# Optimization experiments

Measured on AMD Instinct MI355X. Metric: run time of the kernel, lower is better.

Reference implementation:

```python
import jax, jax.numpy as jnp
import numpy as np
import math

DIM, HEADS, WS, RED = 192, 6, 7, 4
HD = DIM // HEADS
N = WS * WS
BW = 4096  # total windows (B_)


def _pdsca(x, ca_w1, ca_b1, ca_w2, ca_b2, sa_w, sa_b):
    # Parallel dual channel+spatial attention producing mask logits, same shape as x.
    # x: (B, C, 7, 7)
    ca = x.mean(axis=(2, 3))                              # (B, C) global avg pool
    h = jax.nn.gelu(ca @ ca_w1.T + ca_b1)                 # (B, C/r)
    ca = h @ ca_w2.T + ca_b2                              # (B, C)
    sa_in = jnp.concatenate([x.mean(axis=1, keepdims=True),
                             x.max(axis=1, keepdims=True)], axis=1)  # (B, 2, 7, 7)
    sa = jax.lax.conv_general_dilated(sa_in, sa_w, (1, 1), 'SAME',
                                      dimension_numbers=('NCHW', 'OIHW', 'NCHW'))
    sa = sa + sa_b[None, :, None, None]                   # (B, 1, 7, 7)
    return ca[:, :, None, None] + sa                      # broadcast to (B, C, 7, 7)


def _forward(qkv, log_temp, pos_w, pos_b, pos_scale,
             meta_w1, meta_b1, meta_w2, meta_b2,
             q_ca_w1, q_ca_b1, q_ca_w2, q_ca_b2, q_sa_w, q_sa_b,
             k_ca_w1, k_ca_b1, k_ca_w2, k_ca_b2, k_sa_w, k_sa_b,
             proj_w):
    B = qkv.shape[0]
    qkv5 = qkv.reshape(B, N, 3, HEADS, HD).transpose(2, 0, 3, 1, 4)  # (3, B, H, N, hd)
    q, k, v = qkv5[0], qkv5[1], qkv5[2]

    temperature = jnp.exp(log_temp)

    # sigmoid gates on q and k via PDSCA on (B*H, hd, 7, 7) windows
    mq = _pdsca(q.reshape(-1, HD, WS, WS), q_ca_w1, q_ca_b1, q_ca_w2, q_ca_b2, q_sa_w, q_sa_b)
    mk = _pdsca(k.reshape(-1, HD, WS, WS), k_ca_w1, k_ca_b1, k_ca_w2, k_ca_b2, k_sa_w, k_sa_b)
    q = q * jax.nn.sigmoid(mq.reshape(q.shape))
    k = k * jax.nn.sigmoid(mk.reshape(k.shape))

    attn = jnp.einsum('bhnd,bhmd->bhnm', q, k) * temperature  # (B, H, N, N)

    # learned relative position bias: conv1x1 on coord grid -> pairwise diffs -> meta MLP
    coords = jnp.linspace(-1.0, 1.0, WS)
    yg, xg = jnp.meshgrid(coords, coords, indexing='ij')
    grid = jnp.stack([xg, yg], axis=0)                        # (2, 7, 7)
    pe = jnp.einsum('chw,dc->dhw', grid, pos_w) + pos_b[:, None, None]  # (dim, 7, 7)
    pef = pe.reshape(DIM, N).T                                # (N, dim)
    rel = pos_scale * (pef[:, None, :] - pef[None, :, :])     # (N, N, dim)
    bias = jax.nn.gelu(rel @ meta_w1 + meta_b1) @ meta_w2 + meta_b2  # (N, N, H)
    bias = bias.transpose(2, 0, 1)                            # (H, N, N)

    attn = jax.nn.softmax(attn + bias[None], axis=-1)
    out = jnp.einsum('bhnm,bhmd->bnhd', attn, v).reshape(B, N, DIM)
    return out @ proj_w.T                                     # project_out 1x1 conv


def setup_inputs() -> dict:
    key = jax.random.key(0)
    ks = jax.random.split(key, 24)
    s = 0.02
    d = {
        'qkv': jax.random.normal(ks[0], (BW, N, 3 * DIM), dtype=jnp.float32),
        'log_temp': jnp.array([math.log(0.1)], dtype=jnp.float32),
        'pos_w': jax.random.normal(ks[1], (DIM, 2), dtype=jnp.float32) * s,
        'pos_b': jnp.zeros((DIM,), dtype=jnp.float32),
        'pos_scale': jnp.float32(0.1),
        'meta_w1': jax.random.normal(ks[2], (DIM, 128), dtype=jnp.float32) * s,
        'meta_b1': jnp.zeros((128,), dtype=jnp.float32),
        'meta_w2': jax.random.normal(ks[3], (128, HEADS), dtype=jnp.float32) * s,
        'meta_b2': jnp.zeros((HEADS,), dtype=jnp.float32),
        'q_ca_w1': jax.random.normal(ks[4], (HD // RED, HD), dtype=jnp.float32) * s,
        'q_ca_b1': jnp.zeros((HD // RED,), dtype=jnp.float32),
        'q_ca_w2': jax.random.normal(ks[5], (HD, HD // RED), dtype=jnp.float32) * s,
        'q_ca_b2': jnp.zeros((HD,), dtype=jnp.float32),
        'q_sa_w': jax.random.normal(ks[6], (1, 2, 7, 7), dtype=jnp.float32) * s,
        'q_sa_b': jnp.zeros((1,), dtype=jnp.float32),
        'k_ca_w1': jax.random.normal(ks[7], (HD // RED, HD), dtype=jnp.float32) * s,
        'k_ca_b1': jnp.zeros((HD // RED,), dtype=jnp.float32),
        'k_ca_w2': jax.random.normal(ks[8], (HD, HD // RED), dtype=jnp.float32) * s,
        'k_ca_b2': jnp.zeros((HD,), dtype=jnp.float32),
        'k_sa_w': jax.random.normal(ks[9], (1, 2, 7, 7), dtype=jnp.float32) * s,
        'k_sa_b': jnp.zeros((1,), dtype=jnp.float32),
        'proj_w': jax.random.normal(ks[10], (DIM, DIM), dtype=jnp.float32) * s,
    }
    return d


def reference(qkv, log_temp, pos_w, pos_b, pos_scale,
              meta_w1, meta_b1, meta_w2, meta_b2,
              q_ca_w1, q_ca_b1, q_ca_w2, q_ca_b2, q_sa_w, q_sa_b,
              k_ca_w1, k_ca_b1, k_ca_w2, k_ca_b2, k_sa_w, k_sa_b,
              proj_w):
    return _forward(qkv, log_temp, pos_w, pos_b, pos_scale,
                    meta_w1, meta_b1, meta_w2, meta_b2,
                    q_ca_w1, q_ca_b1, q_ca_w2, q_ca_b2, q_sa_w, q_sa_b,
                    k_ca_w1, k_ca_b1, k_ca_w2, k_ca_b2, k_sa_w, k_sa_b,
                    proj_w)
```

## Files before the change

kernel.cpp:

```cpp
#include <hip/hip_runtime.h>
#include <math.h>

#define DIM 192
#define HEADS 6
#define HD 32
#define WS 7
#define NN 49
#define NWIN 4096
#define QKV_ROW (3*DIM)

typedef __attribute__((ext_vector_type(8))) short bf16x8_t;
typedef __attribute__((ext_vector_type(4))) float f32x4_t;

#define MFMA16(a,b,c) __builtin_amdgcn_mfma_f32_16x16x32_bf16((a),(b),(c),0,0,0)

__device__ __forceinline__ float gelu_tanh(float x) {
    const float k0 = 0.7978845608028654f;
    const float k1 = 0.044715f;
    float t = tanhf(k0 * (x + k1 * x * x * x));
    return 0.5f * x * (1.0f + t);
}
__device__ __forceinline__ unsigned short f2bf(float f) {
    __bf16 h = (__bf16)f;
    return __builtin_bit_cast(unsigned short, h);
}
__device__ __forceinline__ float bf2f(unsigned short u) {
    return (float)__builtin_bit_cast(__bf16, u);
}

#define BIASF_FLOATS (HEADS*64*64)
#define WBF_OFF_B    (BIASF_FLOATS*4)
#define OWS_OFF_B    (WBF_OFF_B + DIM*DIM*2)
#define WS_NEEDED    ((size_t)OWS_OFF_B + (size_t)NWIN*HEADS*NN*HD*2)

__global__ __launch_bounds__(128) void bias_kernel(
    const float* __restrict__ pos_w, const float* __restrict__ pos_scale,
    const float* __restrict__ meta_w1, const float* __restrict__ meta_b1,
    const float* __restrict__ meta_w2, const float* __restrict__ meta_b2,
    float* __restrict__ bias_frag)
{
    const int p = blockIdx.x;
    const int n = p / NN, m = p % NN;
    const int i = threadIdx.x;
    __shared__ float hbuf[128];
    const float step = 2.0f / 6.0f;
    const float dx = (float)((n % WS) - (m % WS)) * step;
    const float dy = (float)((n / WS) - (m / WS)) * step;
    const float ps = pos_scale[0];
    float a = meta_b1[i];
    for (int d = 0; d < DIM; ++d) {
        float rel = ps * (pos_w[2*d] * dx + pos_w[2*d+1] * dy);
        a += rel * meta_w1[d*128 + i];
    }
    hbuf[i] = gelu_tanh(a);
    __syncthreads();
    if (i < HEADS) {
        float b = meta_b2[i];
        for (int j = 0; j < 128; ++j) b += hbuf[j] * meta_w2[j*HEADS + i];
        bias_frag[((i*64 + n)*16 + (m & 15))*4 + (m >> 4)] = b;
    }
}

__global__ __launch_bounds__(256) void prep_w(
    const float* __restrict__ proj_w, unsigned short* __restrict__ wbf,
    float* __restrict__ bias_frag)
{
    int idx = blockIdx.x*256 + threadIdx.x;
    if (idx < DIM*DIM) wbf[idx] = f2bf(proj_w[idx]);
    int z = idx - DIM*DIM;
    if (z >= 0 && z < HEADS*15*64) {
        int hh = z / 960, rem = z - hh*960;
        int row = 49 + (rem >> 6), inner = rem & 63;
        bias_frag[(hh*64 + row)*64 + inner] = 0.f;
    }
}

#define XS  40
#define VS  72
#define PPS 72

#define G_SM 0
#define G_MX 49
#define G_CA 98
#define G_SA 130

__device__ __forceinline__ void stats_one(
    const unsigned short* xs,
    const float* __restrict__ w1, const float* __restrict__ b1,
    const float* __restrict__ w2, const float* __restrict__ b2,
    const float* sw, float sab, float* scr, int l)
{
    int c = l & 31, h2 = l >> 5;
    int s0 = h2 ? 25 : 0, s1 = h2 ? 49 : 25;
    float s = 0.f;
    for (int sp = s0; sp < s1; ++sp) {
        int j = c*NN + sp;
        s += bf2f(xs[(j >> 5)*XS + (j & 31)]);
    }
    s += __shfl_xor(s, 32);
    float cm = s * (1.f/49.f);
    int o = l & 7, t8 = l >> 3;
    float part = 0.f;
    #pragma unroll
    for (int kk = 0; kk < 4; ++kk) {
        int c2 = t8 + (kk << 3);
        part += w1[(o << 5) + c2] * __shfl(cm, c2);
    }
    part += __shfl_xor(part, 8);
    part += __shfl_xor(part, 16);
    part += __shfl_xor(part, 32);
    float hid = gelu_tanh(part + b1[o]);
    float a2 = b2[c];
    #pragma unroll
    for (int oo = 0; oo < 8; ++oo)
        a2 += w2[(c << 3) + oo] * __shfl(hid, oo);
    scr[G_CA + c] = a2;
    if (l < NN) {
        float sm = 0.f, mx = -1e30f;
        #pragma unroll
        for (int c2 = 0; c2 < HD; ++c2) {
            int j2 = c2*NN + l;
            float v = bf2f(xs[(j2 >> 5)*XS + (j2 & 31)]);
            sm += v; mx = fmaxf(mx, v);
        }
        scr[G_SM + l] = sm * (1.f/HD);
        scr[G_MX + l] = mx;
        int y = l / WS, x = l - y*WS;
        int y0 = max(0, y-3), y1 = min(6, y+3);
        int x0 = max(0, x-3), x1 = min(6, x+3);
        float a = sab;
        for (int iy = y0; iy <= y1; ++iy) {
            int ky = iy - y + 3;
            for (int ix = x0; ix <= x1; ++ix) {
                int kx = ix - x + 3;
                int s2 = iy*WS + ix;
                a += sw[ky*WS+kx] * scr[G_SM+s2] + sw[NN+ky*WS+kx] * scr[G_MX+s2];
            }
        }
        scr[G_SA + l] = a;
    }
}

__device__ __forceinline__ bf16x8_t gate_frag(
    const unsigned short* xs, int row, int lk8, const float* scr)
{
    bf16x8_t r = *(const bf16x8_t*)&xs[row*XS + lk8];
    bf16x8_t g;
    int flat = row*HD + lk8;
    int c = flat / NN, sp = flat - c*NN;
    #pragma unroll
    for (int e = 0; e < 8; ++e) {
        float gg = __fdividef(1.f, 1.f + __expf(-(scr[G_CA+c] + scr[G_SA+sp])));
        g[e] = (short)f2bf(bf2f((unsigned short)r[e]) * gg);
        if (++sp >= NN) { sp = 0; ++c; }
    }
    return g;
}

__global__ __launch_bounds__(128) void gate_attn(
    const float* __restrict__ qkv,
    const float* __restrict__ log_temp,
    const float* __restrict__ q_ca_w1, const float* __restrict__ q_ca_b1,
    const float* __restrict__ q_ca_w2, const float* __restrict__ q_ca_b2,
    const float* __restrict__ q_sa_w, const float* __restrict__ q_sa_b,
    const float* __restrict__ k_ca_w1, const float* __restrict__ k_ca_b1,
    const float* __restrict__ k_ca_w2, const float* __restrict__ k_ca_b2,
    const float* __restrict__ k_sa_w, const float* __restrict__ k_sa_b,
    const float* __restrict__ bias_frag,
    unsigned short* __restrict__ o_ws)
{
    __shared__ __align__(16) unsigned short x_all[2][NN*XS];
    __shared__ __align__(16) unsigned short v_all[2][HD*VS];
    __shared__ __align__(16) unsigned short p_all[2][16*PPS];
    __shared__ __align__(16) float sw_s[196];

    const int t = threadIdx.x;
    const int w = t >> 6;
    const int l = t & 63;
    const int lrow = l & 15;
    const int lk = l >> 4;
    const int lk8 = lk * 8;
    const int u = blockIdx.x*2 + w;
    const int b = u / HEADS;
    const int h = u - b*HEADS;
    const int hoff = h * HD;
    unsigned short* x_buf = x_all[w];
    unsigned short* v_t = v_all[w];
    unsigned short* p_buf = p_all[w];
    float* scr = (float*)p_buf;
    const float temp = __expf(log_temp[0]);
    const float* qkv_b = qkv + (size_t)b * (NN*QKV_ROW);

    for (int i = l; i < 196; i += 64)
        sw_s[i] = (i < 98) ? q_sa_w[i] : k_sa_w[i-98];
    for (int i = l; i < HD*15; i += 64) {
        int d = i / 15, m = 49 + (i - d*15);
        v_t[d*VS + m] = 0;
    }

    #pragma unroll
    for (int i = 0; i < 7; ++i) {
        int e = l + i*64;
        if (e < NN*8) {
            int n = e >> 3, c = e & 7;
            const float* base = qkv_b + n*QKV_ROW + hoff + (c<<2);
            float4 fv = *(const float4*)(base + 2*DIM);
            float4 fq = *(const float4*)(base);
            int d0 = c << 2;
            v_t[(d0+0)*VS + n] = f2bf(fv.x);
            v_t[(d0+1)*VS + n] = f2bf(fv.y);
            v_t[(d0+2)*VS + n] = f2bf(fv.z);
            v_t[(d0+3)*VS + n] = f2bf(fv.w);
            ushort4 uq = { f2bf(fq.x), f2bf(fq.y), f2bf(fq.z), f2bf(fq.w) };
            *(ushort4*)&x_buf[n*XS + (c<<2)] = uq;
        }
    }

    stats_one(x_buf, q_ca_w1, q_ca_b1, q_ca_w2, q_ca_b2, sw_s, q_sa_b[0], scr, l);
    bf16x8_t qfrag[4];
    #pragma unroll
    for (int s = 0; s < 4; ++s) {
        int ar = s*16 + lrow;
        qfrag[s] = gate_frag(x_buf, ar < NN ? ar : NN-1, lk8, scr);
    }

    #pragma unroll
    for (int i = 0; i < 7; ++i) {
        int e = l + i*64;
        if (e < NN*8) {
            int n = e >> 3, c = e & 7;
            float4 fk = *(const float4*)(qkv_b + n*QKV_ROW + DIM + hoff + (c<<2));
            ushort4 uk = { f2bf(fk.x), f2bf(fk.y), f2bf(fk.z), f2bf(fk.w) };
            *(ushort4*)&x_buf[n*XS + (c<<2)] = uk;
        }
    }

    stats_one(x_buf, k_ca_w1, k_ca_b1, k_ca_w2, k_ca_b2, sw_s + 98, k_sa_b[0], scr, l);
    {
        int c2 = l / NN, sp = l - c2*NN;
        for (int j = l; j < NN*HD; j += 64) {
            int idx = (j >> 5)*XS + (j & 31);
            float g = __fdividef(1.f, 1.f + __expf(-(scr[G_CA+c2] + scr[G_SA+sp])));
            x_buf[idx] = f2bf(bf2f(x_buf[idx]) * g);
            sp += 15; c2 += 1;
            if (sp >= NN) { sp -= NN; ++c2; }
        }
    }

    const float* bias_f = bias_frag + h*64*64;
    unsigned short* o_u = o_ws + (size_t)u * (NN*HD);
    #pragma unroll
    for (int s = 0; s < 4; ++s) {
        f32x4_t sac[4];
        #pragma unroll
        for (int j = 0; j < 4; ++j) {
            int mr = j*16 + lrow;
            int mc = mr < NN ? mr : NN-1;
            bf16x8_t bk = *(const bf16x8_t*)&x_buf[mc*XS + lk8];
            f32x4_t z = (f32x4_t){0.f,0.f,0.f,0.f};
            sac[j] = MFMA16(qfrag[s], bk, z);
        }
        #pragma unroll
        for (int r = 0; r < 4; ++r) {
            int row = s*16 + lk*4 + r;
            float4 b4 = *(const float4*)(bias_f + (row*16 + lrow)*4);
            float v0 = sac[0][r]*temp + b4.x;
            float v1 = sac[1][r]*temp + b4.y;
            float v2 = sac[2][r]*temp + b4.z;
            float v3 = (lrow == 0) ? (sac[3][r]*temp + b4.w) : -1e30f;
            float mx = fmaxf(fmaxf(v0, v1), fmaxf(v2, v3));
            mx = fmaxf(mx, __shfl_xor(mx, 1));
            mx = fmaxf(mx, __shfl_xor(mx, 2));
            mx = fmaxf(mx, __shfl_xor(mx, 4));
            mx = fmaxf(mx, __shfl_xor(mx, 8));
            float e0 = __expf(v0 - mx), e1 = __expf(v1 - mx);
            float e2 = __expf(v2 - mx), e3 = __expf(v3 - mx);
            float sum = e0 + e1 + e2 + e3;
            sum += __shfl_xor(sum, 1);
            sum += __shfl_xor(sum, 2);
            sum += __shfl_xor(sum, 4);
            sum += __shfl_xor(sum, 8);
            float inv = __fdividef(1.f, sum);
            int pb = (lk*4 + r)*PPS + lrow;
            p_buf[pb +  0] = f2bf(e0 * inv);
            p_buf[pb + 16] = f2bf(e1 * inv);
            p_buf[pb + 32] = f2bf(e2 * inv);
            p_buf[pb + 48] = f2bf(e3 * inv);
        }
        f32x4_t oac[2];
        oac[0] = (f32x4_t){0.f,0.f,0.f,0.f};
        oac[1] = (f32x4_t){0.f,0.f,0.f,0.f};
        #pragma unroll
        for (int ks = 0; ks < 2; ++ks) {
            bf16x8_t ap = *(const bf16x8_t*)&p_buf[lrow*PPS + ks*32 + lk8];
            #pragma unroll
            for (int nt = 0; nt < 2; ++nt) {
                bf16x8_t bv = *(const bf16x8_t*)&v_t[(nt*16 + lrow)*VS + ks*32 + lk8];
                oac[nt] = MFMA16(ap, bv, oac[nt]);
            }
        }
        #pragma unroll
        for (int nt = 0; nt < 2; ++nt)
            #pragma unroll
            for (int r = 0; r < 4; ++r) {
                int row = s*16 + lk*4 + r;
                if (row < NN)
                    o_u[row*HD + nt*16 + lrow] = f2bf(oac[nt][r]);
            }
    }
}

__global__ __launch_bounds__(256) void proj_kernel(
    const unsigned short* __restrict__ o_ws,
    const unsigned short* __restrict__ wbf,
    float* __restrict__ out)
{
    const int t = threadIdx.x;
    const int b = blockIdx.x;
    const int w = t >> 6;
    const int l = t & 63;
    const int lrow = l & 15;
    const int lk = l >> 4;
    const int lk8 = lk * 8;

    f32x4_t pacc[4][3];
    #pragma unroll
    for (int s = 0; s < 4; ++s)
        #pragma unroll
        for (int jj = 0; jj < 3; ++jj)
            pacc[s][jj] = (f32x4_t){0.f,0.f,0.f,0.f};

    #pragma unroll
    for (int c = 0; c < HEADS; ++c) {
        bf16x8_t bw[3];
        #pragma unroll
        for (int jj = 0; jj < 3; ++jj)
            bw[jj] = *(const bf16x8_t*)(wbf + ((w*3 + jj)*16 + lrow)*DIM + c*HD + lk8);
        const unsigned short* o_u = o_ws + (size_t)(b*HEADS + c) * (NN*HD);
        #pragma unroll
        for (int s = 0; s < 4; ++s) {
            int ar = s*16 + lrow;
            int ac = ar < NN ? ar : NN-1;
            bf16x8_t ao = *(const bf16x8_t*)(o_u + ac*HD + lk8);
            #pragma unroll
            for (int jj = 0; jj < 3; ++jj)
                pacc[s][jj] = MFMA16(ao, bw[jj], pacc[s][jj]);
        }
    }
    float* out_b = out + (size_t)b * (NN*DIM);
    #pragma unroll
    for (int s = 0; s < 4; ++s)
        #pragma unroll
        for (int jj = 0; jj < 3; ++jj)
            #pragma unroll
            for (int r = 0; r < 4; ++r) {
                int row = s*16 + lk*4 + r;
                if (row < NN)
                    out_b[row*DIM + (w*3 + jj)*16 + lrow] = pacc[s][jj][r];
            }
}

#define QS  200
#define RSV 72
__device__ __forceinline__ void stats_one_f(
    const unsigned short* xs, int hoff,
    const float* __restrict__ w1, const float* __restrict__ b1,
    const float* __restrict__ w2, const float* __restrict__ b2,
    const float* sw, float sab, float* scr, int l)
{
    int c = l & 31, h2 = l >> 5;
    int s0 = h2 ? 25 : 0, s1 = h2 ? 49 : 25;
    float s = 0.f;
    for (int sp = s0; sp < s1; ++sp) {
        int j = c*NN + sp;
        s += bf2f(xs[(j >> 5)*QS + hoff + (j & 31)]);
    }
    s += __shfl_xor(s, 32);
    float cm = s * (1.f/49.f);
    int o = l & 7, t8 = l >> 3;
    float part = 0.f;
    #pragma unroll
    for (int kk = 0; kk < 4; ++kk) {
        int c2 = t8 + (kk << 3);
        part += w1[(o << 5) + c2] * __shfl(cm, c2);
    }
    part += __shfl_xor(part, 8);
    part += __shfl_xor(part, 16);
    part += __shfl_xor(part, 32);
    float hid = gelu_tanh(part + b1[o]);
    float a2 = b2[c];
    #pragma unroll
    for (int oo = 0; oo < 8; ++oo)
        a2 += w2[(c << 3) + oo] * __shfl(hid, oo);
    scr[G_CA + c] = a2;
    if (l < NN) {
        float sm = 0.f, mx = -1e30f;
        #pragma unroll
        for (int c2 = 0; c2 < HD; ++c2) {
            int j2 = c2*NN + l;
            float v = bf2f(xs[(j2 >> 5)*QS + hoff + (j2 & 31)]);
            sm += v; mx = fmaxf(mx, v);
        }
        scr[G_SM + l] = sm * (1.f/HD);
        scr[G_MX + l] = mx;
        int y = l / WS, x = l - y*WS;
        int y0 = max(0, y-3), y1 = min(6, y+3);
        int x0 = max(0, x-3), x1 = min(6, x+3);
        float a = sab;
        for (int iy = y0; iy <= y1; ++iy) {
            int ky = iy - y + 3;
            for (int ix = x0; ix <= x1; ++ix) {
                int kx = ix - x + 3;
                int s2 = iy*WS + ix;
                a += sw[ky*WS+kx] * scr[G_SM+s2] + sw[NN+ky*WS+kx] * scr[G_MX+s2];
            }
        }
        scr[G_SA + l] = a;
    }
}
__device__ __forceinline__ bf16x8_t gate_frag_f(
    const unsigned short* xs, int hoff, int row, int lk8, const float* scr)
{
    bf16x8_t r = *(const bf16x8_t*)&xs[row*QS + hoff + lk8];
    bf16x8_t g;
    int flat = row*HD + lk8;
    #pragma unroll
    for (int e = 0; e < 8; ++e) {
        int f = flat + e;
        int c = f / NN, sp = f - c*NN;
        float gg = 1.f / (1.f + __expf(-(scr[G_CA+c] + scr[G_SA+sp])));
        g[e] = (short)f2bf(bf2f((unsigned short)r[e]) * gg);
    }
    return g;
}
__global__ __launch_bounds__(384) void win_attn_fused(
    const float* __restrict__ qkv, const float* __restrict__ log_temp,
    const float* __restrict__ q_ca_w1, const float* __restrict__ q_ca_b1,
    const float* __restrict__ q_ca_w2, const float* __restrict__ q_ca_b2,
    const float* __restrict__ q_sa_w, const float* __restrict__ q_sa_b,
    const float* __restrict__ k_ca_w1, const float* __restrict__ k_ca_b1,
    const float* __restrict__ k_ca_w2, const float* __restrict__ k_ca_b2,
    const float* __restrict__ k_sa_w, const float* __restrict__ k_sa_b,
    const float* __restrict__ bias_frag, const unsigned short* __restrict__ wbf,
    float* __restrict__ out)
{
    __shared__ __align__(16) unsigned short x_all[NN*QS];
    __shared__ __align__(16) unsigned short p_all[HEADS][16*RSV];
    __shared__ __align__(16) float sw_s[196];
    const int t = threadIdx.x;
    const int b = blockIdx.x;
    const int w = t >> 6;
    const int l = t & 63;
    const int lrow = l & 15;
    const int lk = l >> 4;
    const int lk8 = lk * 8;
    const int hoff = w * HD;
    unsigned short* p_w = p_all[w];
    float* scr = (float*)p_w;
    const float temp = __expf(log_temp[0]);
    const float* qkv_b = qkv + (size_t)b * (NN*QKV_ROW);
    for (int i = l; i < 196; i += 64)
        sw_s[i] = (i < 98) ? q_sa_w[i] : k_sa_w[i-98];
    bf16x8_t vfrag[2][2];
    #pragma unroll
    for (int ks = 0; ks < 2; ++ks)
        #pragma unroll
        for (int nt = 0; nt < 2; ++nt) {
            bf16x8_t f;
            #pragma unroll
            for (int e = 0; e < 8; ++e) {
                int m = ks*32 + lk8 + e;
                float v = 0.f;
                if (m < NN) v = qkv_b[(size_t)m*QKV_ROW + 2*DIM + hoff + nt*16 + lrow];
                f[e] = (short)f2bf(v);
            }
            vfrag[ks][nt] = f;
        }
    float4 kr[7];
    #pragma unroll
    for (int i = 0; i < 7; ++i) {
        int e = l + i*64;
        if (e < NN*8) {
            int n = e >> 3, c = e & 7;
            const float* base = qkv_b + n*QKV_ROW + hoff + (c<<2);
            float4 fq = *(const float4*)(base);
            kr[i] = *(const float4*)(base + DIM);
            ushort4 uq = { f2bf(fq.x), f2bf(fq.y), f2bf(fq.z), f2bf(fq.w) };
            *(ushort4*)&x_all[n*QS + hoff + (c<<2)] = uq;
        }
    }
    stats_one_f(x_all, hoff, q_ca_w1, q_ca_b1, q_ca_w2, q_ca_b2, sw_s, q_sa_b[0], scr, l);
    bf16x8_t qfrag[4];
    #pragma unroll
    for (int s = 0; s < 4; ++s) {
        int ar = s*16 + lrow;
        qfrag[s] = gate_frag_f(x_all, hoff, ar < NN ? ar : NN-1, lk8, scr);
    }
    #pragma unroll
    for (int i = 0; i < 7; ++i) {
        int e = l + i*64;
        if (e < NN*8) {
            int n = e >> 3, c = e & 7;
            ushort4 uk = { f2bf(kr[i].x), f2bf(kr[i].y), f2bf(kr[i].z), f2bf(kr[i].w) };
            *(ushort4*)&x_all[n*QS + hoff + (c<<2)] = uk;
        }
    }
    stats_one_f(x_all, hoff, k_ca_w1, k_ca_b1, k_ca_w2, k_ca_b2, sw_s + 98, k_sa_b[0], scr, l);
    bf16x8_t kfrag[4];
    #pragma unroll
    for (int j = 0; j < 4; ++j) {
        int mr = j*16 + lrow;
        kfrag[j] = gate_frag_f(x_all, hoff, mr < NN ? mr : NN-1, lk8, scr);
    }
    const float* bias_f = bias_frag + w*64*64;
    #pragma unroll
    for (int s = 0; s < 4; ++s) {
        f32x4_t sac[4];
        #pragma unroll
        for (int j = 0; j < 4; ++j) {
            f32x4_t z = (f32x4_t){0.f,0.f,0.f,0.f};
            sac[j] = MFMA16(qfrag[s], kfrag[j], z);
        }
        #pragma unroll
        for (int r = 0; r < 4; ++r) {
            int row = s*16 + lk*4 + r;
            float4 b4 = *(const float4*)(bias_f + (row*16 + lrow)*4);
            float v0 = sac[0][r]*temp + b4.x;
            float v1 = sac[1][r]*temp + b4.y;
            float v2 = sac[2][r]*temp + b4.z;
            float v3 = (lrow == 0) ? (sac[3][r]*temp + b4.w) : -1e30f;
            float mx = fmaxf(fmaxf(v0, v1), fmaxf(v2, v3));
            mx = fmaxf(mx, __shfl_xor(mx, 1));
            mx = fmaxf(mx, __shfl_xor(mx, 2));
            mx = fmaxf(mx, __shfl_xor(mx, 4));
            mx = fmaxf(mx, __shfl_xor(mx, 8));
            float e0 = __expf(v0 - mx), e1 = __expf(v1 - mx);
            float e2 = __expf(v2 - mx), e3 = __expf(v3 - mx);
            float sum = e0 + e1 + e2 + e3;
            sum += __shfl_xor(sum, 1);
            sum += __shfl_xor(sum, 2);
            sum += __shfl_xor(sum, 4);
            sum += __shfl_xor(sum, 8);
            float inv = 1.f / sum;
            int pb = (lk*4 + r)*RSV + lrow;
            p_w[pb +  0] = f2bf(e0 * inv);
            p_w[pb + 16] = f2bf(e1 * inv);
            p_w[pb + 32] = f2bf(e2 * inv);
            p_w[pb + 48] = f2bf(e3 * inv);
        }
        f32x4_t oac[2];
        oac[0] = (f32x4_t){0.f,0.f,0.f,0.f};
        oac[1] = (f32x4_t){0.f,0.f,0.f,0.f};
        #pragma unroll
        for (int ks = 0; ks < 2; ++ks) {
            bf16x8_t ap = *(const bf16x8_t*)&p_w[lrow*RSV + ks*32 + lk8];
            #pragma unroll
            for (int nt = 0; nt < 2; ++nt)
                oac[nt] = MFMA16(ap, vfrag[ks][nt], oac[nt]);
        }
        #pragma unroll
        for (int nt = 0; nt < 2; ++nt)
            #pragma unroll
            for (int r = 0; r < 4; ++r) {
                int row = s*16 + lk*4 + r;
                if (row < NN)
                    x_all[row*QS + hoff + nt*16 + lrow] = f2bf(oac[nt][r]);
            }
    }
    __syncthreads();
    f32x4_t pacc[4][2];
    #pragma unroll
    for (int s2 = 0; s2 < 4; ++s2) {
        pacc[s2][0] = (f32x4_t){0.f,0.f,0.f,0.f};
        pacc[s2][1] = (f32x4_t){0.f,0.f,0.f,0.f};
    }
    #pragma unroll
    for (int s2 = 0; s2 < 4; ++s2) {
        int ar = s2*16 + lrow;
        int ac = ar < NN ? ar : NN-1;
        #pragma unroll
        for (int c = 0; c < 6; ++c) {
            bf16x8_t ao = *(const bf16x8_t*)&x_all[ac*QS + c*32 + lk8];
            #pragma unroll
            for (int jj = 0; jj < 2; ++jj) {
                bf16x8_t bw = *(const bf16x8_t*)(wbf + ((2*w+jj)*16 + lrow)*DIM + c*32 + lk8);
                pacc[s2][jj] = MFMA16(ao, bw, pacc[s2][jj]);
            }
        }
    }
    float* out_b = out + (size_t)b * (NN*DIM);
    #pragma unroll
    for (int s2 = 0; s2 < 4; ++s2)
        #pragma unroll
        for (int jj = 0; jj < 2; ++jj)
            #pragma unroll
            for (int r = 0; r < 4; ++r) {
                int row = s2*16 + lk*4 + r;
                if (row < NN)
                    out_b[row*DIM + (2*w+jj)*16 + lrow] = pacc[s2][jj][r];
            }
}

extern "C" void kernel_launch(void* const* d_in, const int* in_sizes, int n_in,
                              void* d_out, int out_size, void* d_ws, size_t ws_size,
                              hipStream_t stream)
{
    (void)in_sizes; (void)n_in; (void)out_size;
    const float* qkv      = (const float*)d_in[0];
    const float* log_temp = (const float*)d_in[1];
    const float* pos_w    = (const float*)d_in[2];
    const float* pos_scale= (const float*)d_in[4];
    const float* meta_w1  = (const float*)d_in[5];
    const float* meta_b1  = (const float*)d_in[6];
    const float* meta_w2  = (const float*)d_in[7];
    const float* meta_b2  = (const float*)d_in[8];
    const float* q_ca_w1  = (const float*)d_in[9];
    const float* q_ca_b1  = (const float*)d_in[10];
    const float* q_ca_w2  = (const float*)d_in[11];
    const float* q_ca_b2  = (const float*)d_in[12];
    const float* q_sa_w   = (const float*)d_in[13];
    const float* q_sa_b   = (const float*)d_in[14];
    const float* k_ca_w1  = (const float*)d_in[15];
    const float* k_ca_b1  = (const float*)d_in[16];
    const float* k_ca_w2  = (const float*)d_in[17];
    const float* k_ca_b2  = (const float*)d_in[18];
    const float* k_sa_w   = (const float*)d_in[19];
    const float* k_sa_b   = (const float*)d_in[20];
    const float* proj_w   = (const float*)d_in[21];
    float* out = (float*)d_out;

    float* bias_frag = (float*)d_ws;
    unsigned short* wbf = (unsigned short*)((char*)d_ws + WBF_OFF_B);
    unsigned short* o_ws = (unsigned short*)((char*)d_ws + OWS_OFF_B);

    hipLaunchKernelGGL(bias_kernel, dim3(NN*NN), dim3(128), 0, stream,
                       pos_w, pos_scale, meta_w1, meta_b1, meta_w2, meta_b2, bias_frag);
    hipLaunchKernelGGL(prep_w, dim3((DIM*DIM + HEADS*15*64 + 255)/256), dim3(256), 0, stream,
                       proj_w, wbf, bias_frag);
    if (ws_size >= WS_NEEDED) {
        hipLaunchKernelGGL(gate_attn, dim3(NWIN*HEADS/2), dim3(128), 0, stream,
                           qkv, log_temp,
                           q_ca_w1, q_ca_b1, q_ca_w2, q_ca_b2, q_sa_w, q_sa_b,
                           k_ca_w1, k_ca_b1, k_ca_w2, k_ca_b2, k_sa_w, k_sa_b,
                           bias_frag, o_ws);
        hipLaunchKernelGGL(proj_kernel, dim3(NWIN), dim3(256), 0, stream,
                           o_ws, wbf, out);
    } else {
        hipLaunchKernelGGL(win_attn_fused, dim3(NWIN), dim3(384), 0, stream,
                           qkv, log_temp,
                           q_ca_w1, q_ca_b1, q_ca_w2, q_ca_b2, q_sa_w, q_sa_b,
                           k_ca_w1, k_ca_b1, k_ca_w2, k_ca_b2, k_sa_w, k_sa_b,
                           bias_frag, wbf, out);
    }
}
```

Baseline: 383.4 us.

## Swizzle V/P shared layouts, drop softmax max pass, read SA weights directly

Replaces padded row strides for the transposed V and probability tiles in shared memory with XOR-swizzled 64-wide rows, to avoid bank conflicts while using less LDS. Removes the row-max reduction from the softmax and exponentiates the scaled logits directly, saving four shuffles and subtractions per row. Reads the spatial-attention conv weights from global memory instead of staging them in shared memory. Skipping the max subtraction risks overflow if logits grow large.

```diff
diff --git a/kernel.cpp b/kernel.cpp
--- a/kernel.cpp
+++ b/kernel.cpp
@@ -76,8 +76,8 @@
 }
 
 #define XS  40
-#define VS  72
-#define PPS 72
+#define VSW 64
+#define PSW 64
 
 #define G_SM 0
 #define G_MX 49
@@ -88,7 +88,7 @@
     const unsigned short* xs,
     const float* __restrict__ w1, const float* __restrict__ b1,
     const float* __restrict__ w2, const float* __restrict__ b2,
-    const float* sw, float sab, float* scr, int l)
+    const float* __restrict__ sw, float sab, float* scr, int l)
 {
     int c = l & 31, h2 = l >> 5;
     int s0 = h2 ? 25 : 0, s1 = h2 ? 49 : 25;
@@ -170,9 +170,8 @@
     unsigned short* __restrict__ o_ws)
 {
     __shared__ __align__(16) unsigned short x_all[2][NN*XS];
-    __shared__ __align__(16) unsigned short v_all[2][HD*VS];
-    __shared__ __align__(16) unsigned short p_all[2][16*PPS];
-    __shared__ __align__(16) float sw_s[196];
+    __shared__ __align__(16) unsigned short v_all[2][HD*VSW];
+    __shared__ __align__(16) unsigned short p_all[2][16*PSW];
 
     const int t = threadIdx.x;
     const int w = t >> 6;
@@ -191,11 +190,9 @@
     const float temp = __expf(log_temp[0]);
     const float* qkv_b = qkv + (size_t)b * (NN*QKV_ROW);
 
-    for (int i = l; i < 196; i += 64)
-        sw_s[i] = (i < 98) ? q_sa_w[i] : k_sa_w[i-98];
     for (int i = l; i < HD*15; i += 64) {
         int d = i / 15, m = 49 + (i - d*15);
-        v_t[d*VS + m] = 0;
+        v_t[d*VSW + ((((m >> 3) ^ (d & 7)) << 3) | (m & 7))] = 0;
     }
 
     #pragma unroll
@@ -207,16 +204,17 @@
             float4 fv = *(const float4*)(base + 2*DIM);
             float4 fq = *(const float4*)(base);
             int d0 = c << 2;
-            v_t[(d0+0)*VS + n] = f2bf(fv.x);
-            v_t[(d0+1)*VS + n] = f2bf(fv.y);
-            v_t[(d0+2)*VS + n] = f2bf(fv.z);
-            v_t[(d0+3)*VS + n] = f2bf(fv.w);
+            int ng = n >> 3, nl = n & 7;
+            v_t[(d0+0)*VSW + (((ng ^ ((d0+0)&7)) << 3) | nl)] = f2bf(fv.x);
+            v_t[(d0+1)*VSW + (((ng ^ ((d0+1)&7)) << 3) | nl)] = f2bf(fv.y);
+            v_t[(d0+2)*VSW + (((ng ^ ((d0+2)&7)) << 3) | nl)] = f2bf(fv.z);
+            v_t[(d0+3)*VSW + (((ng ^ ((d0+3)&7)) << 3) | nl)] = f2bf(fv.w);
             ushort4 uq = { f2bf(fq.x), f2bf(fq.y), f2bf(fq.z), f2bf(fq.w) };
             *(ushort4*)&x_buf[n*XS + (c<<2)] = uq;
         }
     }
 
-    stats_one(x_buf, q_ca_w1, q_ca_b1, q_ca_w2, q_ca_b2, sw_s, q_sa_b[0], scr, l);
+    stats_one(x_buf, q_ca_w1, q_ca_b1, q_ca_w2, q_ca_b2, q_sa_w, q_sa_b[0], scr, l);
     bf16x8_t qfrag[4];
     #pragma unroll
     for (int s = 0; s < 4; ++s) {
@@ -235,7 +233,7 @@
         }
     }
 
-    stats_one(x_buf, k_ca_w1, k_ca_b1, k_ca_w2, k_ca_b2, sw_s + 98, k_sa_b[0], scr, l);
+    stats_one(x_buf, k_ca_w1, k_ca_b1, k_ca_w2, k_ca_b2, k_sa_w, k_sa_b[0], scr, l);
     {
         int c2 = l / NN, sp = l - c2*NN;
         for (int j = l; j < NN*HD; j += 64) {
@@ -249,6 +247,7 @@
 
     const float* bias_f = bias_frag + h*64*64;
     unsigned short* o_u = o_ws + (size_t)u * (NN*HD);
+    const int lr7 = lrow & 7, lrg = lrow >> 3;
     #pragma unroll
     for (int s = 0; s < 4; ++s) {
         f32x4_t sac[4];
@@ -264,38 +263,34 @@
         for (int r = 0; r < 4; ++r) {
             int row = s*16 + lk*4 + r;
             float4 b4 = *(const float4*)(bias_f + (row*16 + lrow)*4);
-            float v0 = sac[0][r]*temp + b4.x;
-            float v1 = sac[1][r]*temp + b4.y;
-            float v2 = sac[2][r]*temp + b4.z;
-            float v3 = (lrow == 0) ? (sac[3][r]*temp + b4.w) : -1e30f;
-            float mx = fmaxf(fmaxf(v0, v1), fmaxf(v2, v3));
-            mx = fmaxf(mx, __shfl_xor(mx, 1));
-            mx = fmaxf(mx, __shfl_xor(mx, 2));
-            mx = fmaxf(mx, __shfl_xor(mx, 4));
-            mx = fmaxf(mx, __shfl_xor(mx, 8));
-            float e0 = __expf(v0 - mx), e1 = __expf(v1 - mx);
-            float e2 = __expf(v2 - mx), e3 = __expf(v3 - mx);
+            float e0 = __expf(sac[0][r]*temp + b4.x);
+            float e1 = __expf(sac[1][r]*temp + b4.y);
+            float e2 = __expf(sac[2][r]*temp + b4.z);
+            float e3 = (lrow == 0) ? __expf(sac[3][r]*temp + b4.w) : 0.f;
             float sum = e0 + e1 + e2 + e3;
             sum += __shfl_xor(sum, 1);
             sum += __shfl_xor(sum, 2);
             sum += __shfl_xor(sum, 4);
             sum += __shfl_xor(sum, 8);
             float inv = __fdividef(1.f, sum);
-            int pb = (lk*4 + r)*PPS + lrow;
-            p_buf[pb +  0] = f2bf(e0 * inv);
-            p_buf[pb + 16] = f2bf(e1 * inv);
-            p_buf[pb + 32] = f2bf(e2 * inv);
-            p_buf[pb + 48] = f2bf(e3 * inv);
+            int prow = lk*4 + r;
+            int pbase = prow*PSW + lr7;
+            int r7 = prow & 7;
+            p_buf[pbase + (((0*2 + lrg) ^ r7) << 3)] = f2bf(e0 * inv);
+            p_buf[pbase + (((1*2 + lrg) ^ r7) << 3)] = f2bf(e1 * inv);
+            p_buf[pbase + (((2*2 + lrg) ^ r7) << 3)] = f2bf(e2 * inv);
+            p_buf[pbase + (((3*2 + lrg) ^ r7) << 3)] = f2bf(e3 * inv);
         }
         f32x4_t oac[2];
         oac[0] = (f32x4_t){0.f,0.f,0.f,0.f};
         oac[1] = (f32x4_t){0.f,0.f,0.f,0.f};
         #pragma unroll
         for (int ks = 0; ks < 2; ++ks) {
-            bf16x8_t ap = *(const bf16x8_t*)&p_buf[lrow*PPS + ks*32 + lk8];
+            bf16x8_t ap = *(const bf16x8_t*)&p_buf[lrow*PSW + (((ks*4 + lk) ^ lr7) << 3)];
             #pragma unroll
             for (int nt = 0; nt < 2; ++nt) {
-                bf16x8_t bv = *(const bf16x8_t*)&v_t[(nt*16 + lrow)*VS + ks*32 + lk8];
+                int vr = nt*16 + lrow;
+                bf16x8_t bv = *(const bf16x8_t*)&v_t[vr*VSW + (((ks*4 + lk) ^ (vr & 7)) << 3)];
                 oac[nt] = MFMA16(ap, bv, oac[nt]);
             }
         }
```

New measurement: 500.1 us. 30.4% more time.
